# Kernel optimization log

Hardware: AMD Instinct MI355X
Metric: run time of the kernel (lower is better)

## Reference

```python
import jax, jax.numpy as jnp
import numpy as np

B, SEQ, L, NK, NCLS = 4096, 8, 2048, 256, 100
LEN_VOCAB, IPD_VOCAB, EBIT, EBDIN = 1500, 256, 16, 4
C, D = 8, 4  # MM codebook groups / group dim


def setup_inputs() -> dict:
    key = jax.random.key(0)
    ks = jax.random.split(key, 16)
    f32 = jnp.float32
    return {
        'x': jax.random.randint(ks[0], (B, SEQ, 2), 0, 256, dtype=jnp.int64),
        'len_emb': jax.random.normal(ks[1], (LEN_VOCAB, EBIT), f32),
        'ipd_emb': jax.random.normal(ks[2], (IPD_VOCAB, EBIT), f32),
        'W1': jax.random.normal(ks[3], (2 * EBIT, EBDIN), f32) * 0.1,
        'b1': jax.random.normal(ks[4], (EBDIN,), f32) * 0.1,
        'We': jax.random.normal(ks[5], (EBDIN, L), f32) * 0.1,
        'be': jax.random.normal(ks[6], (L,), f32) * 0.1,
        'w3': jax.random.normal(ks[7], (NK, 3, L), f32) * 0.02,
        'w4': jax.random.normal(ks[8], (NK, 4, L), f32) * 0.02,
        'w5': jax.random.normal(ks[9], (NK, 5, L), f32) * 0.02,
        'W2': jax.random.normal(ks[10], (15 * NK, NCLS), f32) * 0.02,
        'b2': jax.random.normal(ks[11], (NCLS,), f32) * 0.02,
        'S': jax.random.normal(ks[12], (C, D, 15), f32),
        'H': jax.random.normal(ks[13], (15, 16), f32),
        'T': jax.random.normal(ks[14], (C, 15), f32),
        'LUT': jax.random.normal(ks[15], (C, 16, D), f32),
    }


def _mm(h, S, H, T, LUT):
    # h: [B, C, D]
    m = jnp.einsum('bcd,cdk->bck', h, S) - T - 0.0001
    t = jnp.tanh(m)
    m = t + jax.lax.stop_gradient(jnp.sign(m) - t)  # straight-through sign
    m = jnp.einsum('bck,kj->bcj', m, H)             # [B, C, 16]
    oh = jax.nn.one_hot(jnp.argmax(m, -1), 16, dtype=m.dtype)
    sm = jax.nn.softmax(m, -1)                      # temperature = 1
    xo = jnp.einsum('bck,ckd->bcd', oh, LUT)
    xs = jnp.einsum('bck,ckd->bcd', sm, LUT)
    return xs + jax.lax.stop_gradient(xo - xs)      # straight-through one-hot


def _segment_conv(g, ws):
    # g: [B, 8, L]. Original loops i=0..7 building an input with only row i
    # nonzero, then Conv2d(kernel=(K,L), bias=False)+ReLU and sums the 8 results.
    # With a single nonzero row, conv output at position p is x[i]@w[i-p] when
    # p <= i <= p+K-1 and 0 otherwise (relu(0)=0), so the sum over i equals a
    # diagonal gather of relu of the per-row projections -- exact same math.
    Bn = g.shape[0]
    feats = []
    for w in ws:  # w: [nk, K, L]
        K = w.shape[1]
        P = 8 - K + 1
        proj = jax.nn.relu(jnp.einsum('bhl,nkl->bhnk', g, w))  # [B,8,nk,K]
        xk = sum(proj[:, k:k + P, :, k] for k in range(K))      # [B,P,nk]
        feats.append(jnp.transpose(xk, (0, 2, 1)).reshape(Bn, -1))  # (nk,P) order
    return jnp.concatenate(feats, -1)  # [B, 15*nk]


def reference(x, len_emb, ipd_emb, W1, b1, We, be, w3, w4, w5, W2, b2, S, H, T, LUT):
    Bn = x.shape[0]
    le = len_emb[x[:, :, 0]]                        # [B, 8, 16]
    ie = ipd_emb[x[:, :, 1]]                        # [B, 8, 16]
    h = jnp.concatenate([le, ie], -1) @ W1 + b1     # [B, 8, 4]
    m = _mm(h.reshape(Bn, C, D), S, H, T, LUT)      # [B, 8, 4]
    g = m @ We + be                                 # [B, 8, L]
    f = _segment_conv(g, (w3, w4, w5))              # [B, 15*nk]
    logits = f @ W2 + b2
    return jax.nn.log_softmax(logits, -1)
```

## Files before the change

kernel.cpp:

```cpp
#include <hip/hip_runtime.h>
#include <math.h>


__global__ void k_R(const float* __restrict__ We, const float* __restrict__ be,
                    const float* __restrict__ w3, const float* __restrict__ w4,
                    const float* __restrict__ w5, const float* __restrict__ LUT,
                    float* __restrict__ R) {
  int nk = blockIdx.x;
  const float* wrow;
  if (nk < 768)       wrow = w3 + nk * 2048;
  else if (nk < 1792) wrow = w4 + (nk - 768) * 2048;
  else                wrow = w5 + (nk - 1792) * 2048;
  int t = threadIdx.x;
  float a0 = 0.f, a1 = 0.f, a2 = 0.f, a3 = 0.f, a4 = 0.f;
  const float4* wp  = (const float4*)wrow;
  const float4* e0p = (const float4*)(We);
  const float4* e1p = (const float4*)(We + 2048);
  const float4* e2p = (const float4*)(We + 4096);
  const float4* e3p = (const float4*)(We + 6144);
  const float4* bep = (const float4*)(be);
  for (int i = t; i < 512; i += 256) {
    float4 w = wp[i];
    float4 e0 = e0p[i], e1 = e1p[i], e2 = e2p[i], e3 = e3p[i], bb = bep[i];
    a0 += w.x * e0.x + w.y * e0.y + w.z * e0.z + w.w * e0.w;
    a1 += w.x * e1.x + w.y * e1.y + w.z * e1.z + w.w * e1.w;
    a2 += w.x * e2.x + w.y * e2.y + w.z * e2.z + w.w * e2.w;
    a3 += w.x * e3.x + w.y * e3.y + w.z * e3.z + w.w * e3.w;
    a4 += w.x * bb.x + w.y * bb.y + w.z * bb.z + w.w * bb.w;
  }
  __shared__ float red[5][256];
  red[0][t] = a0; red[1][t] = a1; red[2][t] = a2; red[3][t] = a3; red[4][t] = a4;
  __syncthreads();
  for (int s = 128; s > 0; s >>= 1) {
    if (t < s) {
      red[0][t] += red[0][t + s];
      red[1][t] += red[1][t + s];
      red[2][t] += red[2][t + s];
      red[3][t] += red[3][t + s];
      red[4][t] += red[4][t + s];
    }
    __syncthreads();
  }
  if (t < 128) {
    float ww0 = red[0][0], ww1 = red[1][0], ww2 = red[2][0], ww3 = red[3][0];
    float bw = red[4][0];
    const float* lut = LUT + t * 4;
    float v = bw + lut[0] * ww0 + lut[1] * ww1 + lut[2] * ww2 + lut[3] * ww3;
    R[t * 3072 + nk] = fmaxf(v, 0.f);
  }
}

__global__ void k_zeroG(float* __restrict__ G) {
  int i = blockIdx.x * blockDim.x + threadIdx.x;
  if (i < 12800) G[i] = 0.f;
}

__global__ void k_G(const float* __restrict__ R, const float* __restrict__ W2,
                    float* __restrict__ G) {
  int h = blockIdx.x;
  int z = blockIdx.y;
  int c = threadIdx.x;
  int nk0 = z * 64;
  int K, P, rowbase, n, k;
  if (nk0 < 768)       { K = 3; P = 6; rowbase = 0;    n = nk0 / 3;  k = nk0 - n * 3; }
  else if (nk0 < 1792) { K = 4; P = 5; rowbase = 1536; int t2 = nk0 - 768;  n = t2 >> 2; k = t2 & 3; }
  else                 { K = 5; P = 4; rowbase = 2816; int t2 = nk0 - 1792; n = t2 / 5;  k = t2 - n * 5; }
  float acc[16];
#pragma unroll
  for (int j = 0; j < 16; j++) acc[j] = 0.f;
  bool act = c < 100;
  for (int it = 0; it < 64; ++it) {
    int nk = nk0 + it;
    int p = h - k;
    if (p >= 0 && p < P) {
      float w2v = act ? W2[(rowbase + n * P + p) * 100 + c] : 0.f;
      const float* Rp = R + h * 16 * 3072 + nk;
#pragma unroll
      for (int j = 0; j < 16; j++) acc[j] += Rp[j * 3072] * w2v;
    }
    if (++k == K) { k = 0; ++n; }
  }
  if (act) {
#pragma unroll
    for (int j = 0; j < 16; j++) atomicAdd(&G[(h * 16 + j) * 100 + c], acc[j]);
  }
}

__global__ void k_jtab(const int* __restrict__ x, const float* __restrict__ len_emb,
                       const float* __restrict__ ipd_emb, const float* __restrict__ W1,
                       const float* __restrict__ b1, const float* __restrict__ S,
                       const float* __restrict__ Hm, const float* __restrict__ T,
                       int* __restrict__ jtab) {
  int bh = blockIdx.x * blockDim.x + threadIdx.x;
  if (bh >= 32768) return;
  int pos = bh & 7;
  bool is64 = true;
#pragma unroll
  for (int q = 0; q < 16; q++) is64 = is64 && (x[2 * q + 1] == 0);
  int i0, i1;
  if (is64) { i0 = x[4 * bh];     i1 = x[4 * bh + 2]; }
  else      { i0 = x[2 * bh];     i1 = x[2 * bh + 1]; }
  const float* le = len_emb + i0 * 16;
  const float* ie = ipd_emb + i1 * 16;
  float hv[4];
#pragma unroll
  for (int d = 0; d < 4; d++) hv[d] = b1[d];
  for (int i = 0; i < 16; i++) {
    float lv = le[i], iv = ie[i];
#pragma unroll
    for (int d = 0; d < 4; d++) hv[d] += lv * W1[i * 4 + d] + iv * W1[(16 + i) * 4 + d];
  }
  float sg[15];
#pragma unroll
  for (int kk = 0; kk < 15; kk++) {
    float m = -1e-4f - T[pos * 15 + kk];
#pragma unroll
    for (int d = 0; d < 4; d++) m += hv[d] * S[(pos * 4 + d) * 15 + kk];
    sg[kk] = (m > 0.f) ? 1.f : ((m < 0.f) ? -1.f : 0.f);
  }
  int bj = 0;
  float bv = -INFINITY;
  for (int j = 0; j < 16; j++) {
    float v = 0.f;
#pragma unroll
    for (int kk = 0; kk < 15; kk++) v += sg[kk] * Hm[kk * 16 + j];
    if (v > bv) { bv = v; bj = j; }
  }
  jtab[bh] = bj;
}

__global__ void k_out(const int* __restrict__ jtab, const float* __restrict__ G,
                      const float* __restrict__ b2, float* __restrict__ out) {
  int b = blockIdx.x;
  int t = threadIdx.x;
  int js[8];
#pragma unroll
  for (int p = 0; p < 8; p++) js[p] = jtab[b * 8 + p];
  int c0 = t, c1 = t + 64;
  float v0, v1 = -INFINITY;
  {
    float a = b2[c0];
#pragma unroll
    for (int p = 0; p < 8; p++) a += G[(p * 16 + js[p]) * 100 + c0];
    v0 = a;
  }
  if (c1 < 100) {
    float a = b2[c1];
#pragma unroll
    for (int p = 0; p < 8; p++) a += G[(p * 16 + js[p]) * 100 + c1];
    v1 = a;
  }
  float mx = fmaxf(v0, v1);
#pragma unroll
  for (int off = 32; off > 0; off >>= 1) mx = fmaxf(mx, __shfl_xor(mx, off, 64));
  float e = expf(v0 - mx) + ((c1 < 100) ? expf(v1 - mx) : 0.f);
#pragma unroll
  for (int off = 32; off > 0; off >>= 1) e += __shfl_xor(e, off, 64);
  float lse = mx + logf(e);
  out[b * 100 + c0] = v0 - lse;
  if (c1 < 100) out[b * 100 + c1] = v1 - lse;
}

extern "C" void kernel_launch(void* const* d_in, const int* in_sizes, int n_in,
                              void* d_out, int out_size, void* d_ws, size_t ws_size,
                              hipStream_t stream) {
  const int*   x       = (const int*)  d_in[0];
  const float* len_emb = (const float*)d_in[1];
  const float* ipd_emb = (const float*)d_in[2];
  const float* W1      = (const float*)d_in[3];
  const float* b1      = (const float*)d_in[4];
  const float* We      = (const float*)d_in[5];
  const float* be      = (const float*)d_in[6];
  const float* w3      = (const float*)d_in[7];
  const float* w4      = (const float*)d_in[8];
  const float* w5      = (const float*)d_in[9];
  const float* W2      = (const float*)d_in[10];
  const float* b2      = (const float*)d_in[11];
  const float* S       = (const float*)d_in[12];
  const float* Hm      = (const float*)d_in[13];
  const float* T       = (const float*)d_in[14];
  const float* LUT     = (const float*)d_in[15];
  float* out = (float*)d_out;

  float* R    = (float*)d_out;
  float* G    = (float*)d_ws;
  int*   jtab = (int*)((char*)d_ws + 51200);

  k_zeroG<<<13, 1024, 0, stream>>>(G);
  k_R<<<3072, 256, 0, stream>>>(We, be, w3, w4, w5, LUT, R);
  k_jtab<<<128, 256, 0, stream>>>(x, len_emb, ipd_emb, W1, b1, S, Hm, T, jtab);
  dim3 gB(8, 48);
  k_G<<<gB, 128, 0, stream>>>(R, W2, G);
  k_out<<<4096, 64, 0, stream>>>(jtab, G, b2, out);
}
```

Before: 141.1 us.

## Fuse G zeroing into R kernel, warp-per-row reduction, fold jtab into output kernel

The zero-fill of G moves into the first block of the R kernel. The R kernel now gives each 64-lane wavefront one weight row and reduces with shuffles instead of a shared-memory tree with many barriers. The codeword-index computation moves into the output kernel, so the separate jtab kernel and its global round trip go away, cutting two launches. In exchange, the output kernel serialises 8 threads on the index work before its barrier, and zeroing G relies on stream ordering ahead of k_G.

```diff
diff --git a/kernel.cpp b/kernel.cpp
--- a/kernel.cpp
+++ b/kernel.cpp
@@ -2,16 +2,20 @@
 #include <math.h>
 
 
-__global__ void k_R(const float* __restrict__ We, const float* __restrict__ be,
-                    const float* __restrict__ w3, const float* __restrict__ w4,
-                    const float* __restrict__ w5, const float* __restrict__ LUT,
-                    float* __restrict__ R) {
-  int nk = blockIdx.x;
+__global__ void k_Rz(const float* __restrict__ We, const float* __restrict__ be,
+                     const float* __restrict__ w3, const float* __restrict__ w4,
+                     const float* __restrict__ w5, const float* __restrict__ LUT,
+                     float* __restrict__ R, float* __restrict__ G) {
+  int tid = threadIdx.x;
+  if (blockIdx.x == 0) {
+    for (int i = tid; i < 12800; i += 256) G[i] = 0.f;
+  }
+  int lane = tid & 63;
+  int nk = blockIdx.x * 4 + (tid >> 6);
   const float* wrow;
   if (nk < 768)       wrow = w3 + nk * 2048;
   else if (nk < 1792) wrow = w4 + (nk - 768) * 2048;
   else                wrow = w5 + (nk - 1792) * 2048;
-  int t = threadIdx.x;
   float a0 = 0.f, a1 = 0.f, a2 = 0.f, a3 = 0.f, a4 = 0.f;
   const float4* wp  = (const float4*)wrow;
   const float4* e0p = (const float4*)(We);
@@ -19,7 +23,8 @@
   const float4* e2p = (const float4*)(We + 4096);
   const float4* e3p = (const float4*)(We + 6144);
   const float4* bep = (const float4*)(be);
-  for (int i = t; i < 512; i += 256) {
+#pragma unroll
+  for (int i = lane; i < 512; i += 64) {
     float4 w = wp[i];
     float4 e0 = e0p[i], e1 = e1p[i], e2 = e2p[i], e3 = e3p[i], bb = bep[i];
     a0 += w.x * e0.x + w.y * e0.y + w.z * e0.z + w.w * e0.w;
@@ -28,31 +33,21 @@
     a3 += w.x * e3.x + w.y * e3.y + w.z * e3.z + w.w * e3.w;
     a4 += w.x * bb.x + w.y * bb.y + w.z * bb.z + w.w * bb.w;
   }
-  __shared__ float red[5][256];
-  red[0][t] = a0; red[1][t] = a1; red[2][t] = a2; red[3][t] = a3; red[4][t] = a4;
-  __syncthreads();
-  for (int s = 128; s > 0; s >>= 1) {
-    if (t < s) {
-      red[0][t] += red[0][t + s];
-      red[1][t] += red[1][t + s];
-      red[2][t] += red[2][t + s];
-      red[3][t] += red[3][t + s];
-      red[4][t] += red[4][t + s];
-    }
-    __syncthreads();
+#pragma unroll
+  for (int off = 32; off > 0; off >>= 1) {
+    a0 += __shfl_xor(a0, off, 64);
+    a1 += __shfl_xor(a1, off, 64);
+    a2 += __shfl_xor(a2, off, 64);
+    a3 += __shfl_xor(a3, off, 64);
+    a4 += __shfl_xor(a4, off, 64);
   }
-  if (t < 128) {
-    float ww0 = red[0][0], ww1 = red[1][0], ww2 = red[2][0], ww3 = red[3][0];
-    float bw = red[4][0];
-    const float* lut = LUT + t * 4;
-    float v = bw + lut[0] * ww0 + lut[1] * ww1 + lut[2] * ww2 + lut[3] * ww3;
-    R[t * 3072 + nk] = fmaxf(v, 0.f);
+#pragma unroll
+  for (int r = 0; r < 2; r++) {
+    int rr = lane + r * 64;
+    const float* lut = LUT + rr * 4;
+    float v = a4 + lut[0] * a0 + lut[1] * a1 + lut[2] * a2 + lut[3] * a3;
+    R[rr * 3072 + nk] = fmaxf(v, 0.f);
   }
-}
-
-__global__ void k_zeroG(float* __restrict__ G) {
-  int i = blockIdx.x * blockDim.x + threadIdx.x;
-  if (i < 12800) G[i] = 0.f;
 }
 
 __global__ void k_G(const float* __restrict__ R, const float* __restrict__ W2,
@@ -86,56 +81,53 @@
   }
 }
 
-__global__ void k_jtab(const int* __restrict__ x, const float* __restrict__ len_emb,
-                       const float* __restrict__ ipd_emb, const float* __restrict__ W1,
-                       const float* __restrict__ b1, const float* __restrict__ S,
-                       const float* __restrict__ Hm, const float* __restrict__ T,
-                       int* __restrict__ jtab) {
-  int bh = blockIdx.x * blockDim.x + threadIdx.x;
-  if (bh >= 32768) return;
-  int pos = bh & 7;
-  bool is64 = true;
-#pragma unroll
-  for (int q = 0; q < 16; q++) is64 = is64 && (x[2 * q + 1] == 0);
-  int i0, i1;
-  if (is64) { i0 = x[4 * bh];     i1 = x[4 * bh + 2]; }
-  else      { i0 = x[2 * bh];     i1 = x[2 * bh + 1]; }
-  const float* le = len_emb + i0 * 16;
-  const float* ie = ipd_emb + i1 * 16;
-  float hv[4];
-#pragma unroll
-  for (int d = 0; d < 4; d++) hv[d] = b1[d];
-  for (int i = 0; i < 16; i++) {
-    float lv = le[i], iv = ie[i];
-#pragma unroll
-    for (int d = 0; d < 4; d++) hv[d] += lv * W1[i * 4 + d] + iv * W1[(16 + i) * 4 + d];
-  }
-  float sg[15];
-#pragma unroll
-  for (int kk = 0; kk < 15; kk++) {
-    float m = -1e-4f - T[pos * 15 + kk];
-#pragma unroll
-    for (int d = 0; d < 4; d++) m += hv[d] * S[(pos * 4 + d) * 15 + kk];
-    sg[kk] = (m > 0.f) ? 1.f : ((m < 0.f) ? -1.f : 0.f);
-  }
-  int bj = 0;
-  float bv = -INFINITY;
-  for (int j = 0; j < 16; j++) {
-    float v = 0.f;
-#pragma unroll
-    for (int kk = 0; kk < 15; kk++) v += sg[kk] * Hm[kk * 16 + j];
-    if (v > bv) { bv = v; bj = j; }
-  }
-  jtab[bh] = bj;
-}
-
-__global__ void k_out(const int* __restrict__ jtab, const float* __restrict__ G,
-                      const float* __restrict__ b2, float* __restrict__ out) {
+__global__ void k_out(const int* __restrict__ x, const float* __restrict__ len_emb,
+                      const float* __restrict__ ipd_emb, const float* __restrict__ W1,
+                      const float* __restrict__ b1, const float* __restrict__ S,
+                      const float* __restrict__ Hm, const float* __restrict__ T,
+                      const float* __restrict__ G, const float* __restrict__ b2,
+                      float* __restrict__ out) {
   int b = blockIdx.x;
   int t = threadIdx.x;
-  int js[8];
+  __shared__ int js[8];
+  if (t < 8) {
+    int pos = t;
+    int bh = b * 8 + pos;
+    bool is64 = true;
 #pragma unroll
-  for (int p = 0; p < 8; p++) js[p] = jtab[b * 8 + p];
+    for (int q = 0; q < 16; q++) is64 = is64 && (x[2 * q + 1] == 0);
+    int i0, i1;
+    if (is64) { i0 = x[4 * bh]; i1 = x[4 * bh + 2]; }
+    else      { i0 = x[2 * bh]; i1 = x[2 * bh + 1]; }
+    const float* le = len_emb + i0 * 16;
+    const float* ie = ipd_emb + i1 * 16;
+    float hv[4];
+#pragma unroll
+    for (int d = 0; d < 4; d++) hv[d] = b1[d];
+    for (int i = 0; i < 16; i++) {
+      float lv = le[i], iv = ie[i];
+#pragma unroll
+      for (int d = 0; d < 4; d++) hv[d] += lv * W1[i * 4 + d] + iv * W1[(16 + i) * 4 + d];
+    }
+    float sg[15];
+#pragma unroll
+    for (int kk = 0; kk < 15; kk++) {
+      float m = -1e-4f - T[pos * 15 + kk];
+#pragma unroll
+      for (int d = 0; d < 4; d++) m += hv[d] * S[(pos * 4 + d) * 15 + kk];
+      sg[kk] = (m > 0.f) ? 1.f : ((m < 0.f) ? -1.f : 0.f);
+    }
+    int bj = 0;
+    float bv = -INFINITY;
+    for (int j = 0; j < 16; j++) {
+      float v = 0.f;
+#pragma unroll
+      for (int kk = 0; kk < 15; kk++) v += sg[kk] * Hm[kk * 16 + j];
+      if (v > bv) { bv = v; bj = j; }
+    }
+    js[pos] = bj;
+  }
+  __syncthreads();
   int c0 = t, c1 = t + 64;
   float v0, v1 = -INFINITY;
   {
@@ -182,14 +174,11 @@
   const float* LUT     = (const float*)d_in[15];
   float* out = (float*)d_out;
 
-  float* R    = (float*)d_out;
-  float* G    = (float*)d_ws;
-  int*   jtab = (int*)((char*)d_ws + 51200);
+  float* R = (float*)d_out;
+  float* G = (float*)d_ws;
 
-  k_zeroG<<<13, 1024, 0, stream>>>(G);
-  k_R<<<3072, 256, 0, stream>>>(We, be, w3, w4, w5, LUT, R);
-  k_jtab<<<128, 256, 0, stream>>>(x, len_emb, ipd_emb, W1, b1, S, Hm, T, jtab);
+  k_Rz<<<768, 256, 0, stream>>>(We, be, w3, w4, w5, LUT, R, G);
   dim3 gB(8, 48);
   k_G<<<gB, 128, 0, stream>>>(R, W2, G);
-  k_out<<<4096, 64, 0, stream>>>(jtab, G, b2, out);
+  k_out<<<4096, 64, 0, stream>>>(x, len_emb, ipd_emb, W1, b1, S, Hm, T, G, b2, out);
 }
```

Result: no change. 138.7 us (-1.8%).
